# Kernel tuning notes

Measured on AMD Instinct MI355X. Metric: run time of the kernel, lower is better.

Reference implementation:

```python
import jax, jax.numpy as jnp
import numpy as np
from jax import lax

B, J, H, W = 64, 17, 96, 96
TOPK = 8


def setup_inputs() -> dict:
    key = jax.random.key(0)
    k1, k2, k3, k4 = jax.random.split(key, 4)
    output_s = jax.random.normal(k1, (B, J, H, W), dtype=jnp.float32)
    output_t = jax.random.normal(k2, (B, J, H, W), dtype=jnp.float32)
    target = jax.random.uniform(k3, (B, J, H, W), dtype=jnp.float32)
    # make half the joints have max(gt) == 1 exactly, to exercise both branches
    target = target.at[:, : J // 2, 0, 0].set(1.0)
    target_weight = jax.random.uniform(k4, (B, J, 1), dtype=jnp.float32)
    return {
        "output_s": output_s,
        "output_t": output_t,
        "target": target,
        "target_weight": target_weight,
        "effective_num_joints": 17,
    }


def reference(output_s, output_t, target, target_weight, effective_num_joints):
    b, j = output_t.shape[0], output_t.shape[1]
    s = output_s.reshape(b, j, -1)  # [B, J, HW]
    t = output_t.reshape(b, j, -1)
    g = target.reshape(b, j, -1)
    w = target_weight  # [B, J, 1] broadcasts over HW

    # per-joint condition: max over batch+pixels of (unweighted) gt == 1
    cond = (jnp.max(g, axis=(0, 2)) == 1.0)  # [J]

    sw, tw, gw = s * w, t * w, g * w
    d_sg = (sw - gw) ** 2  # [B, J, HW]
    d_st = (sw - tw) ** 2

    # elementwise per-joint loss, then mean over pixels -> [B, J]
    per = 0.5 * jnp.where(cond[None, :, None], d_sg, d_sg + d_st)
    loss_mat = per.mean(axis=2)  # [B, J]

    # OHKM: per-sample top-k over joints, averaged
    topk_vals, _ = lax.top_k(loss_mat, TOPK)  # [B, k]
    ohkm_loss_s = jnp.mean(jnp.sum(topk_vals, axis=1) / TOPK)

    # accumulated mean-MSE over joints
    m_sg = d_sg.mean(axis=(0, 2))  # [J]
    m_st = d_st.mean(axis=(0, 2))
    mse_loss_s = jnp.sum(jnp.where(cond, m_sg, m_sg + m_st))

    final_loss = ohkm_loss_s + mse_loss_s
    return (ohkm_loss_s, mse_loss_s / effective_num_joints, final_loss)
```

## Files before the change

### kernel.cpp

```cpp
#include <hip/hip_runtime.h>
#include <math.h>

#define NB 64
#define NJ 17
#define HW 9216
#define NBJ (NB * NJ)
#define TOPK_K 8
#define NSEG 3
#define SEG_F4 (HW / 4 / NSEG)
#define BLK 256
#define F4_PER_THR (SEG_F4 / BLK)
#define NBLOCKS (NBJ * NSEG)
#define NCNT 32
#define CNT_STRIDE 32
#define WS_OFF 1024

__global__ __launch_bounds__(BLK) void fused_kernel(
    const float* __restrict__ s,
    const float* __restrict__ t,
    const float* __restrict__ g,
    const float* __restrict__ w,
    const int* __restrict__ enj_p,
    float* __restrict__ out,
    float* __restrict__ ws_raw)
{
    unsigned int* cnt = (unsigned int*)ws_raw;
    float* ws = ws_raw + WS_OFF;

    __shared__ float sh_ssg[NBJ];
    __shared__ float sh_sst[NBJ];
    __shared__ float sh_mgA[NBJ];
    __shared__ float cond_sh[NJ];
    __shared__ float msum_sh[NJ];

    if (blockIdx.x < NBLOCKS) {
        const int bj  = blockIdx.x / NSEG;
        const int seg = blockIdx.x % NSEG;
        const size_t base4 = (size_t)bj * (HW / 4) + (size_t)seg * SEG_F4;
        const float4* __restrict__ s4 = (const float4*)s + base4;
        const float4* __restrict__ t4 = (const float4*)t + base4;
        const float4* __restrict__ g4 = (const float4*)g + base4;

        float4 a[F4_PER_THR], b[F4_PER_THR], c[F4_PER_THR];
        #pragma unroll
        for (int k = 0; k < F4_PER_THR; ++k) a[k] = s4[threadIdx.x + k * BLK];
        #pragma unroll
        for (int k = 0; k < F4_PER_THR; ++k) b[k] = t4[threadIdx.x + k * BLK];
        #pragma unroll
        for (int k = 0; k < F4_PER_THR; ++k) c[k] = g4[threadIdx.x + k * BLK];

        float ssg = 0.f, sst = 0.f, mg = -INFINITY;

        #define ACCUM(av, bv, cv)                                \
            {                                                    \
                float d1 = (av) - (cv), d2 = (av) - (bv);        \
                ssg += d1 * d1; sst += d2 * d2;                  \
                mg = fmaxf(mg, (cv));                            \
            }

        #pragma unroll
        for (int k = 0; k < F4_PER_THR; ++k) {
            ACCUM(a[k].x, b[k].x, c[k].x)
            ACCUM(a[k].y, b[k].y, c[k].y)
            ACCUM(a[k].z, b[k].z, c[k].z)
            ACCUM(a[k].w, b[k].w, c[k].w)
        }
        #undef ACCUM

        #pragma unroll
        for (int off = 32; off > 0; off >>= 1) {
            ssg += __shfl_down(ssg, off);
            sst += __shfl_down(sst, off);
            mg = fmaxf(mg, __shfl_down(mg, off));
        }

        __shared__ float sh_sg[4], sh_st[4], sh_mg4[4];
        const int wave = threadIdx.x >> 6;
        const int lane = threadIdx.x & 63;
        if (lane == 0) { sh_sg[wave] = ssg; sh_st[wave] = sst; sh_mg4[wave] = mg; }
        __syncthreads();

        if (threadIdx.x == 0) {
            const float fsg = (sh_sg[0] + sh_sg[1]) + (sh_sg[2] + sh_sg[3]);
            const float fst = (sh_st[0] + sh_st[1]) + (sh_st[2] + sh_st[3]);
            const float fmg = fmaxf(fmaxf(sh_mg4[0], sh_mg4[1]),
                                    fmaxf(sh_mg4[2], sh_mg4[3]));
            __hip_atomic_store(&ws[(0 * NSEG + seg) * NBJ + bj], fsg,
                               __ATOMIC_RELAXED, __HIP_MEMORY_SCOPE_AGENT);
            __hip_atomic_store(&ws[(1 * NSEG + seg) * NBJ + bj], fst,
                               __ATOMIC_RELAXED, __HIP_MEMORY_SCOPE_AGENT);
            __hip_atomic_store(&ws[(2 * NSEG + seg) * NBJ + bj], fmg,
                               __ATOMIC_RELAXED, __HIP_MEMORY_SCOPE_AGENT);
            asm volatile("s_waitcnt vmcnt(0)" ::: "memory");
            unsigned int* my_cnt = cnt + (blockIdx.x & (NCNT - 1)) * CNT_STRIDE;
            __hip_atomic_fetch_add(my_cnt, 1u, __ATOMIC_RELAXED,
                                   __HIP_MEMORY_SCOPE_AGENT);
        }
        return;
    }

    const int tid = threadIdx.x;
    if (tid == 0) {
        unsigned total;
        do {
            total = 0;
            #pragma unroll
            for (int i = 0; i < NCNT; ++i)
                total += __hip_atomic_load(cnt + i * CNT_STRIDE,
                                           __ATOMIC_RELAXED,
                                           __HIP_MEMORY_SCOPE_AGENT);
            if (total < (unsigned)NBLOCKS) __builtin_amdgcn_s_sleep(8);
        } while (total < (unsigned)NBLOCKS);
    }
    __syncthreads();

    for (int i = tid; i < NBJ; i += BLK) {
        float fsg = 0.f, fst = 0.f, fmg = -INFINITY;
        #pragma unroll
        for (int sg2 = 0; sg2 < NSEG; ++sg2) {
            fsg += __hip_atomic_load(&ws[(0 * NSEG + sg2) * NBJ + i],
                                     __ATOMIC_RELAXED, __HIP_MEMORY_SCOPE_AGENT);
            fst += __hip_atomic_load(&ws[(1 * NSEG + sg2) * NBJ + i],
                                     __ATOMIC_RELAXED, __HIP_MEMORY_SCOPE_AGENT);
            fmg = fmaxf(fmg,
                  __hip_atomic_load(&ws[(2 * NSEG + sg2) * NBJ + i],
                                     __ATOMIC_RELAXED, __HIP_MEMORY_SCOPE_AGENT));
        }
        const float wv = w[i];
        const float w2 = wv * wv;
        sh_ssg[i] = fsg * w2;
        sh_sst[i] = fst * w2;
        sh_mgA[i] = fmg;
    }
    __syncthreads();

    if (tid < NJ * 8) {
        const int j = tid >> 3;
        const int sub = tid & 7;
        float fsg = 0.f, fst = 0.f, fmg = -INFINITY;
        for (int bb = sub; bb < NB; bb += 8) {
            fsg += sh_ssg[bb * NJ + j];
            fst += sh_sst[bb * NJ + j];
            fmg = fmaxf(fmg, sh_mgA[bb * NJ + j]);
        }
        #pragma unroll
        for (int off = 4; off > 0; off >>= 1) {
            fsg += __shfl_down(fsg, off);
            fst += __shfl_down(fst, off);
            fmg = fmaxf(fmg, __shfl_down(fmg, off));
        }
        if (sub == 0) {
            const bool cond = (fmg == 1.0f);
            cond_sh[j] = cond ? 1.f : 0.f;
            const float inv_bhw = 1.f / (float)(NB * HW);
            msum_sh[j] = cond ? (fsg * inv_bhw) : ((fsg + fst) * inv_bhw);
        }
    }
    __syncthreads();

    if (tid < NB) {
        float lm[NJ];
        const float inv_hw = 1.f / (float)HW;
        #pragma unroll
        for (int j = 0; j < NJ; ++j) {
            const float fsg = sh_ssg[tid * NJ + j];
            const float fst = sh_sst[tid * NJ + j];
            const float v = (cond_sh[j] != 0.f) ? fsg : (fsg + fst);
            lm[j] = 0.5f * v * inv_hw;
        }
        float tk = 0.f;
        for (int k = 0; k < TOPK_K; ++k) {
            int mi = 0;
            float mv = lm[0];
            #pragma unroll
            for (int j = 1; j < NJ; ++j) {
                if (lm[j] > mv) { mv = lm[j]; mi = j; }
            }
            tk += mv;
            #pragma unroll
            for (int j = 0; j < NJ; ++j) {
                if (j == mi) lm[j] = -INFINITY;
            }
        }
        #pragma unroll
        for (int off = 32; off > 0; off >>= 1) tk += __shfl_down(tk, off);

        if (tid == 0) {
            const float ohkm = tk / (float)(TOPK_K * NB);
            float mse = 0.f;
            for (int j = 0; j < NJ; ++j) mse += msum_sh[j];
            const float enj = (float)(*enj_p);
            out[0] = ohkm;
            out[1] = mse / enj;
            out[2] = ohkm + mse;
        }
    }
}

extern "C" void kernel_launch(void* const* d_in, const int* in_sizes, int n_in,
                              void* d_out, int out_size, void* d_ws, size_t ws_size,
                              hipStream_t stream) {
    const float* output_s = (const float*)d_in[0];
    const float* output_t = (const float*)d_in[1];
    const float* target   = (const float*)d_in[2];
    const float* tweight  = (const float*)d_in[3];
    const int*   enj      = (const int*)d_in[4];
    float* out = (float*)d_out;
    float* ws  = (float*)d_ws;

    hipMemsetAsync(d_ws, 0, WS_OFF * sizeof(float), stream);
    fused_kernel<<<NBLOCKS + 1, BLK, 0, stream>>>(output_s, output_t, target,
                                                  tweight, enj, out, ws);
}
```

Before: 148.1 us.

## Process four slices per block with double-buffered register prefetch

Each block now handles four consecutive segments instead of one, so the grid shrinks from 3264 to 816 reducer blocks. While one slice is being reduced, the next slice's s/t/g values are loaded into a second register buffer. Per-slice partials are written to shared memory and stored with a single counter increment per block. The workspace is reindexed to match. This cuts block launch and tail overhead and keeps more loads in flight, but it doubles register use, which may lower occupancy.

```diff
diff --git a/kernel.cpp b/kernel.cpp
--- a/kernel.cpp
+++ b/kernel.cpp
@@ -6,11 +6,12 @@
 #define HW 9216
 #define NBJ (NB * NJ)
 #define TOPK_K 8
-#define NSEG 3
-#define SEG_F4 (HW / 4 / NSEG)
+#define SEG_F4 (HW / 4 / 3)
+#define NSLICE (NBJ * 3)
 #define BLK 256
-#define F4_PER_THR (SEG_F4 / BLK)
-#define NBLOCKS (NBJ * NSEG)
+#define F4T (SEG_F4 / BLK)
+#define SPB 4
+#define NBLOCKS (NSLICE / SPB)
 #define NCNT 32
 #define CNT_STRIDE 32
 #define WS_OFF 1024
@@ -34,63 +35,83 @@
     __shared__ float msum_sh[NJ];
 
     if (blockIdx.x < NBLOCKS) {
-        const int bj  = blockIdx.x / NSEG;
-        const int seg = blockIdx.x % NSEG;
-        const size_t base4 = (size_t)bj * (HW / 4) + (size_t)seg * SEG_F4;
-        const float4* __restrict__ s4 = (const float4*)s + base4;
-        const float4* __restrict__ t4 = (const float4*)t + base4;
-        const float4* __restrict__ g4 = (const float4*)g + base4;
-
-        float4 a[F4_PER_THR], b[F4_PER_THR], c[F4_PER_THR];
-        #pragma unroll
-        for (int k = 0; k < F4_PER_THR; ++k) a[k] = s4[threadIdx.x + k * BLK];
-        #pragma unroll
-        for (int k = 0; k < F4_PER_THR; ++k) b[k] = t4[threadIdx.x + k * BLK];
-        #pragma unroll
-        for (int k = 0; k < F4_PER_THR; ++k) c[k] = g4[threadIdx.x + k * BLK];
-
-        float ssg = 0.f, sst = 0.f, mg = -INFINITY;
-
-        #define ACCUM(av, bv, cv)                                \
-            {                                                    \
-                float d1 = (av) - (cv), d2 = (av) - (bv);        \
-                ssg += d1 * d1; sst += d2 * d2;                  \
-                mg = fmaxf(mg, (cv));                            \
-            }
-
-        #pragma unroll
-        for (int k = 0; k < F4_PER_THR; ++k) {
-            ACCUM(a[k].x, b[k].x, c[k].x)
-            ACCUM(a[k].y, b[k].y, c[k].y)
-            ACCUM(a[k].z, b[k].z, c[k].z)
-            ACCUM(a[k].w, b[k].w, c[k].w)
-        }
-        #undef ACCUM
-
-        #pragma unroll
-        for (int off = 32; off > 0; off >>= 1) {
-            ssg += __shfl_down(ssg, off);
-            sst += __shfl_down(sst, off);
-            mg = fmaxf(mg, __shfl_down(mg, off));
-        }
-
-        __shared__ float sh_sg[4], sh_st[4], sh_mg4[4];
+        const int s0 = blockIdx.x * SPB;
+        const size_t tb = (size_t)s0 * SEG_F4 + threadIdx.x;
+        const float4* __restrict__ s4 = (const float4*)s;
+        const float4* __restrict__ t4 = (const float4*)t;
+        const float4* __restrict__ g4 = (const float4*)g;
+
+        __shared__ float red[SPB][3][4];
         const int wave = threadIdx.x >> 6;
         const int lane = threadIdx.x & 63;
-        if (lane == 0) { sh_sg[wave] = ssg; sh_st[wave] = sst; sh_mg4[wave] = mg; }
+
+        float4 A[2][F4T], Bv[2][F4T], C[2][F4T];
+        #pragma unroll
+        for (int k = 0; k < F4T; ++k) A[0][k]  = s4[tb + k * BLK];
+        #pragma unroll
+        for (int k = 0; k < F4T; ++k) Bv[0][k] = t4[tb + k * BLK];
+        #pragma unroll
+        for (int k = 0; k < F4T; ++k) C[0][k]  = g4[tb + k * BLK];
+
+        #pragma unroll
+        for (int j = 0; j < SPB; ++j) {
+            const int cur = j & 1, nxt = cur ^ 1;
+            if (j + 1 < SPB) {
+                const size_t nb = tb + (size_t)(j + 1) * SEG_F4;
+                #pragma unroll
+                for (int k = 0; k < F4T; ++k) A[nxt][k]  = s4[nb + k * BLK];
+                #pragma unroll
+                for (int k = 0; k < F4T; ++k) Bv[nxt][k] = t4[nb + k * BLK];
+                #pragma unroll
+                for (int k = 0; k < F4T; ++k) C[nxt][k]  = g4[nb + k * BLK];
+            }
+
+            float ssg = 0.f, sst = 0.f, mg = -INFINITY;
+            #define ACCUM(av, bv, cv)                            \
+                {                                                \
+                    float d1 = (av) - (cv), d2 = (av) - (bv);    \
+                    ssg += d1 * d1; sst += d2 * d2;              \
+                    mg = fmaxf(mg, (cv));                        \
+                }
+            #pragma unroll
+            for (int k = 0; k < F4T; ++k) {
+                ACCUM(A[cur][k].x, Bv[cur][k].x, C[cur][k].x)
+                ACCUM(A[cur][k].y, Bv[cur][k].y, C[cur][k].y)
+                ACCUM(A[cur][k].z, Bv[cur][k].z, C[cur][k].z)
+                ACCUM(A[cur][k].w, Bv[cur][k].w, C[cur][k].w)
+            }
+            #undef ACCUM
+
+            #pragma unroll
+            for (int off = 32; off > 0; off >>= 1) {
+                ssg += __shfl_down(ssg, off);
+                sst += __shfl_down(sst, off);
+                mg = fmaxf(mg, __shfl_down(mg, off));
+            }
+            if (lane == 0) {
+                red[j][0][wave] = ssg;
+                red[j][1][wave] = sst;
+                red[j][2][wave] = mg;
+            }
+        }
+
         __syncthreads();
-
         if (threadIdx.x == 0) {
-            const float fsg = (sh_sg[0] + sh_sg[1]) + (sh_sg[2] + sh_sg[3]);
-            const float fst = (sh_st[0] + sh_st[1]) + (sh_st[2] + sh_st[3]);
-            const float fmg = fmaxf(fmaxf(sh_mg4[0], sh_mg4[1]),
-                                    fmaxf(sh_mg4[2], sh_mg4[3]));
-            __hip_atomic_store(&ws[(0 * NSEG + seg) * NBJ + bj], fsg,
-                               __ATOMIC_RELAXED, __HIP_MEMORY_SCOPE_AGENT);
-            __hip_atomic_store(&ws[(1 * NSEG + seg) * NBJ + bj], fst,
-                               __ATOMIC_RELAXED, __HIP_MEMORY_SCOPE_AGENT);
-            __hip_atomic_store(&ws[(2 * NSEG + seg) * NBJ + bj], fmg,
-                               __ATOMIC_RELAXED, __HIP_MEMORY_SCOPE_AGENT);
+            #pragma unroll
+            for (int j = 0; j < SPB; ++j) {
+                const float fsg = (red[j][0][0] + red[j][0][1]) +
+                                  (red[j][0][2] + red[j][0][3]);
+                const float fst = (red[j][1][0] + red[j][1][1]) +
+                                  (red[j][1][2] + red[j][1][3]);
+                const float fmg = fmaxf(fmaxf(red[j][2][0], red[j][2][1]),
+                                        fmaxf(red[j][2][2], red[j][2][3]));
+                __hip_atomic_store(&ws[0 * NSLICE + s0 + j], fsg,
+                                   __ATOMIC_RELAXED, __HIP_MEMORY_SCOPE_AGENT);
+                __hip_atomic_store(&ws[1 * NSLICE + s0 + j], fst,
+                                   __ATOMIC_RELAXED, __HIP_MEMORY_SCOPE_AGENT);
+                __hip_atomic_store(&ws[2 * NSLICE + s0 + j], fmg,
+                                   __ATOMIC_RELAXED, __HIP_MEMORY_SCOPE_AGENT);
+            }
             asm volatile("s_waitcnt vmcnt(0)" ::: "memory");
             unsigned int* my_cnt = cnt + (blockIdx.x & (NCNT - 1)) * CNT_STRIDE;
             __hip_atomic_fetch_add(my_cnt, 1u, __ATOMIC_RELAXED,
@@ -117,13 +138,13 @@
     for (int i = tid; i < NBJ; i += BLK) {
         float fsg = 0.f, fst = 0.f, fmg = -INFINITY;
         #pragma unroll
-        for (int sg2 = 0; sg2 < NSEG; ++sg2) {
-            fsg += __hip_atomic_load(&ws[(0 * NSEG + sg2) * NBJ + i],
+        for (int k = 0; k < 3; ++k) {
+            fsg += __hip_atomic_load(&ws[0 * NSLICE + 3 * i + k],
                                      __ATOMIC_RELAXED, __HIP_MEMORY_SCOPE_AGENT);
-            fst += __hip_atomic_load(&ws[(1 * NSEG + sg2) * NBJ + i],
+            fst += __hip_atomic_load(&ws[1 * NSLICE + 3 * i + k],
                                      __ATOMIC_RELAXED, __HIP_MEMORY_SCOPE_AGENT);
             fmg = fmaxf(fmg,
-                  __hip_atomic_load(&ws[(2 * NSEG + sg2) * NBJ + i],
+                  __hip_atomic_load(&ws[2 * NSLICE + 3 * i + k],
                                      __ATOMIC_RELAXED, __HIP_MEMORY_SCOPE_AGENT));
         }
         const float wv = w[i];
```

Result: no change. 150.2 us (+1.4%).
